# Kernel tuning notes

Hardware: AMD Instinct MI355X
Metric: run time of the kernel (lower is better)

## Reference

```python
import jax, jax.numpy as jnp
import numpy as np
import math

NB_STEPS = 50  # matches init kwarg nb_steps


def cc_quadrature(nb_steps):
    # Clenshaw-Curtis weights/nodes, identical to UMNN's compute_cc_weights.
    lam = np.arange(nb_steps + 1, dtype=np.float64).reshape(-1, 1)
    lam = np.cos((lam @ lam.T) * math.pi / nb_steps)
    lam[:, 0] = 0.5
    lam[:, -1] = 0.5 * lam[:, -1]
    lam = lam * 2.0 / nb_steps
    W = np.arange(nb_steps + 1, dtype=np.float64).reshape(-1, 1)
    W[np.arange(1, nb_steps + 1, 2)] = 0
    W = 2.0 / (1.0 - W ** 2)
    W[0] = 1
    W[np.arange(1, nb_steps + 1, 2)] = 0
    cc_weights = (lam.T @ W).astype(np.float32)                 # [K, 1]
    steps = np.cos(np.arange(nb_steps + 1, dtype=np.float64).reshape(-1, 1)
                   * math.pi / nb_steps).astype(np.float32)     # [K, 1]
    return jnp.asarray(cc_weights), jnp.asarray(steps)


def integrand_mlp(xh, W1, b1, W2, b2, W3, b3, W4, b4):
    y = jax.nn.relu(jnp.einsum('bkd,hd->bkh', xh, W1) + b1)
    y = jax.nn.relu(jnp.einsum('bkh,gh->bkg', y, W2) + b2)
    y = jax.nn.relu(jnp.einsum('bkg,fg->bkf', y, W3) + b3)
    y = jnp.einsum('bkf,of->bko', y, W4) + b4
    return jax.nn.elu(y) + 1.0


def setup_inputs() -> dict:
    key = jax.random.key(0)
    ks = jax.random.split(key, 10)
    B, HD, IN_D = 16384, 128, 64
    x = jax.random.normal(ks[0], (B, 1), dtype=jnp.float32)
    h = jax.random.normal(ks[1], (B, IN_D - 1), dtype=jnp.float32)
    def lin(k, fan_out, fan_in):
        return jax.random.normal(k, (fan_out, fan_in), dtype=jnp.float32) / np.sqrt(fan_in)
    return {
        'x': x, 'h': h,
        'W1': lin(ks[2], HD, IN_D), 'b1': jax.random.normal(ks[3], (HD,), dtype=jnp.float32) * 0.01,
        'W2': lin(ks[4], HD, HD),   'b2': jax.random.normal(ks[5], (HD,), dtype=jnp.float32) * 0.01,
        'W3': lin(ks[6], HD, HD),   'b3': jax.random.normal(ks[7], (HD,), dtype=jnp.float32) * 0.01,
        'W4': lin(ks[8], 1, HD),    'b4': jax.random.normal(ks[9], (1,), dtype=jnp.float32) * 0.01,
    }


def reference(x, h, W1, b1, W2, b2, W3, b3, W4, b4):
    cc_w, steps = cc_quadrature(NB_STEPS)          # [K,1], [K,1]
    xmax = jnp.max(x) + 10.0
    x0 = x                                          # [B,1]
    xT = jnp.zeros_like(x) + xmax                   # xfinal broadcast
    # quadrature points X_steps: [B, K, 1]
    X = x0[:, None, :] + (xT - x0)[:, None, :] * (steps[None, :, :] + 1.0) * 0.5
    B, K = X.shape[0], X.shape[1]
    hK = jnp.broadcast_to(h[:, None, :], (B, K, h.shape[1]))
    xh = jnp.concatenate([X, hK], axis=-1)          # [B, K, in_d]
    f = integrand_mlp(xh, W1, b1, W2, b2, W3, b3, W4, b4)  # [B, K, 1]
    z = jnp.sum(f * cc_w[None, :, :], axis=1)       # [B, 1]
    return z * (xT - x0) * 0.5
```

## Files before the change

### kernel.cpp

```cpp
#include <hip/hip_runtime.h>
#include <hip/hip_bf16.h>
#include <math.h>


#define B_N    16384
#define KQ     51
#define HD     128
#define IND    64
#define BLK    128
#define GRID   512
#define RPB    32
#define RPW    16
#define SPW    (RPW * KQ)
#define TPW    (SPW / 16)

typedef __attribute__((ext_vector_type(8))) short short8;
typedef __attribute__((ext_vector_type(4))) float f32x4;

union S8U { short8 s8; unsigned u[4]; };

__device__ __forceinline__ unsigned short f2bf(float f) {
    __hip_bfloat16 t = __float2bfloat16(f);
    return *reinterpret_cast<unsigned short*>(&t);
}

#if defined(__gfx950__) && defined(__has_builtin)
#if __has_builtin(__builtin_amdgcn_cvt_pk_bf16_f32)
#define HAVE_PK_BF16 1
#endif
#endif

__device__ __forceinline__ unsigned pk_bf16(float lo, float hi) {
#ifdef HAVE_PK_BF16
    typedef __attribute__((ext_vector_type(2))) __bf16 bfv2;
    bfv2 r = __builtin_amdgcn_cvt_pk_bf16_f32(lo, hi);
    return *reinterpret_cast<unsigned*>(&r);
#else
    return (unsigned)f2bf(lo) | ((unsigned)f2bf(hi) << 16);
#endif
}

__launch_bounds__(BLK, 1)
__global__ void umnn_fused(const float* __restrict__ x,  const float* __restrict__ h,
                           const float* __restrict__ W1, const float* __restrict__ b1,
                           const float* __restrict__ W2, const float* __restrict__ b2,
                           const float* __restrict__ W3, const float* __restrict__ b3,
                           const float* __restrict__ W4, const float* __restrict__ b4,
                           float* __restrict__ out)
{
    __shared__ __align__(16) float hpL[RPB * HD];
    __shared__ __align__(16) char  y2x[2][4096];
    __shared__ __align__(16) float hshT[63 * 36];
    __shared__ float vs[2][SPW + 16];
    __shared__ float xL[RPB];
    __shared__ float sSteps[KQ], sCcw[KQ];
    __shared__ float red2[2];

    const int tid  = threadIdx.x;
    const int w    = tid >> 6;
    const int lane = tid & 63;
    const int q    = lane >> 4;
    const int lm   = lane & 15;
    const int swz  = lm & 7;
    const int rowBase = blockIdx.x * RPB;

    if (tid < KQ) {
        const int j = tid;
        const float pi50 = 0.06283185307179586f;
        sSteps[j] = __cosf((float)j * pi50);
        float s = 0.0f;
        for (int i = 0; i <= 50; i += 2) {
            float Wi = (i == 0) ? 1.0f : 2.0f / (1.0f - (float)(i * i));
            float lam;
            if (j == 0) lam = 0.5f;
            else {
                int mp = (i * j) % 100;
                lam = __cosf((float)mp * pi50);
                if (j == 50) lam *= 0.5f;
            }
            s += (lam * 0.04f) * Wi;
        }
        sCcw[j] = s;
    }
    {
        const f32x4* x4 = (const f32x4*)x;
        float mx = -1e30f;
        for (int i = tid; i < B_N / 4; i += BLK) {
            f32x4 v = x4[i];
            mx = fmaxf(fmaxf(mx, fmaxf(v[0], v[1])), fmaxf(v[2], v[3]));
        }
        #pragma unroll
        for (int d = 32; d > 0; d >>= 1) mx = fmaxf(mx, __shfl_xor(mx, d));
        if (lane == 0) red2[w] = mx;
    }
    for (int i = tid; i < RPB * 63; i += BLK) {
        int r = i / 63, d = i - r * 63;
        hshT[d * 36 + r] = h[(rowBase) * 63 + i];
    }
    if (tid < RPB) xL[tid] = x[rowBase + tid];
    __syncthreads();

    const float xmax = fmaxf(red2[0], red2[1]) + 10.0f;

    {
        const int n = tid;
        float acc[RPB];
        const float b1v = b1[n];
        #pragma unroll
        for (int r = 0; r < RPB; ++r) acc[r] = b1v;
        const float* wr = W1 + n * IND + 1;
        #pragma unroll 1
        for (int d = 0; d < IND - 1; ++d) {
            float wv = wr[d];
            const float* ht = hshT + d * 36;
            #pragma unroll
            for (int rc = 0; rc < RPB / 4; ++rc) {
                f32x4 hv = *(const f32x4*)(ht + rc * 4);
                acc[rc * 4 + 0] = fmaf(wv, hv[0], acc[rc * 4 + 0]);
                acc[rc * 4 + 1] = fmaf(wv, hv[1], acc[rc * 4 + 1]);
                acc[rc * 4 + 2] = fmaf(wv, hv[2], acc[rc * 4 + 2]);
                acc[rc * 4 + 3] = fmaf(wv, hv[3], acc[rc * 4 + 3]);
            }
        }
        #pragma unroll
        for (int r = 0; r < RPB; ++r) hpL[r * HD + n] = acc[r];
    }

    float w1x[32];
    #pragma unroll
    for (int kk = 0; kk < 4; ++kk)
        #pragma unroll
        for (int j = 0; j < 8; ++j)
            w1x[kk * 8 + j] = W1[(kk * 32 + q * 8 + j) * IND];

    short8 W2A[8][4], W3A[8][4];
    f32x4  b2c[8], b3c[8], W4c[8];
    #pragma unroll
    for (int nt = 0; nt < 8; ++nt) {
        #pragma unroll
        for (int kk = 0; kk < 4; ++kk) {
            const float* p2 = W2 + (nt * 16 + lm) * HD + kk * 32 + q * 8;
            const float* p3 = W3 + (nt * 16 + lm) * HD + kk * 32 + q * 8;
            S8U a2, a3;
            #pragma unroll
            for (int j = 0; j < 4; ++j) {
                a2.u[j] = pk_bf16(p2[2 * j], p2[2 * j + 1]);
                a3.u[j] = pk_bf16(p3[2 * j], p3[2 * j + 1]);
            }
            W2A[nt][kk] = a2.s8; W3A[nt][kk] = a3.s8;
        }
        b2c[nt] = *(const f32x4*)(b2 + nt * 16 + q * 4);
        b3c[nt] = *(const f32x4*)(b3 + nt * 16 + q * 4);
        W4c[nt] = *(const f32x4*)(W4 + nt * 16 + q * 4);
    }
    const float b4v = b4[0];
    char*  myY2 = y2x[w];
    float* vsW  = vs[w];
    __syncthreads();

    const int S0 = blockIdx.x * (RPB * KQ) + w * SPW;

    auto computeY1 = [&](int tt, short8* Y) {
        const int s   = S0 + tt * 16 + lm;
        const unsigned row = (unsigned)s / KQ;
        const int k   = s - (int)row * KQ;
        const int rl  = min((int)row - rowBase, RPB - 1);
        const float x0 = xL[rl];
        const float X  = fmaf((xmax - x0) * 0.5f, sSteps[k] + 1.0f, x0);
        #pragma unroll
        for (int kk = 0; kk < 4; ++kk) {
            const float* hp = hpL + rl * HD + kk * 32 + q * 8;
            f32x4 ha = *(const f32x4*)hp;
            f32x4 hb = *(const f32x4*)(hp + 4);
            S8U u;
            u.u[0] = pk_bf16(fmaxf(fmaf(X, w1x[kk*8+0], ha[0]), 0.f),
                             fmaxf(fmaf(X, w1x[kk*8+1], ha[1]), 0.f));
            u.u[1] = pk_bf16(fmaxf(fmaf(X, w1x[kk*8+2], ha[2]), 0.f),
                             fmaxf(fmaf(X, w1x[kk*8+3], ha[3]), 0.f));
            u.u[2] = pk_bf16(fmaxf(fmaf(X, w1x[kk*8+4], hb[0]), 0.f),
                             fmaxf(fmaf(X, w1x[kk*8+5], hb[1]), 0.f));
            u.u[3] = pk_bf16(fmaxf(fmaf(X, w1x[kk*8+6], hb[2]), 0.f),
                             fmaxf(fmaf(X, w1x[kk*8+7], hb[3]), 0.f));
            Y[kk] = u.s8;
        }
    };

    short8 Y1c[4], Y1n[4];
    computeY1(0, Y1c);

    #pragma unroll 1
    for (int tt = 0; tt < TPW; ++tt) {
        f32x4 C[8];
        #pragma unroll
        for (int nt = 0; nt < 8; ++nt) C[nt] = b2c[nt];
        #pragma unroll
        for (int kk = 0; kk < 4; ++kk)
            #pragma unroll
            for (int nt = 0; nt < 8; ++nt)
                C[nt] = __builtin_amdgcn_mfma_f32_16x16x32_bf16(W2A[nt][kk], Y1c[kk], C[nt], 0, 0, 0);

        #pragma unroll
        for (int nt = 0; nt < 8; ++nt) {
            unsigned lo = pk_bf16(fmaxf(C[nt][0], 0.f), fmaxf(C[nt][1], 0.f));
            unsigned hi = pk_bf16(fmaxf(C[nt][2], 0.f), fmaxf(C[nt][3], 0.f));
            *(int2*)(myY2 + lm * 256 + (((2*nt + (q>>1)) ^ swz) << 4) + ((q & 1) << 3))
                = make_int2((int)lo, (int)hi);
        }

        computeY1(tt + 1, Y1n);

        short8 Y2[4];
        #pragma unroll
        for (int kk = 0; kk < 4; ++kk)
            Y2[kk] = *(const short8*)(myY2 + lm * 256 + (((kk*4 + q) ^ swz) << 4));

        #pragma unroll
        for (int nt = 0; nt < 8; ++nt) C[nt] = b3c[nt];
        #pragma unroll
        for (int kk = 0; kk < 4; ++kk)
            #pragma unroll
            for (int nt = 0; nt < 8; ++nt)
                C[nt] = __builtin_amdgcn_mfma_f32_16x16x32_bf16(W3A[nt][kk], Y2[kk], C[nt], 0, 0, 0);

        float p = 0.f;
        #pragma unroll
        for (int nt = 0; nt < 8; ++nt) {
            p = fmaf(fmaxf(C[nt][0], 0.f), W4c[nt][0], p);
            p = fmaf(fmaxf(C[nt][1], 0.f), W4c[nt][1], p);
            p = fmaf(fmaxf(C[nt][2], 0.f), W4c[nt][2], p);
            p = fmaf(fmaxf(C[nt][3], 0.f), W4c[nt][3], p);
        }
        p += __shfl_xor(p, 16);
        p += __shfl_xor(p, 32);
        if (lane < 16) vsW[tt * 16 + lm] = p;

        #pragma unroll
        for (int kk = 0; kk < 4; ++kk) Y1c[kk] = Y1n[kk];
    }

    {
        const int r   = lane >> 2;
        const int sub = lane & 3;
        float a = 0.f;
        #pragma unroll 1
        for (int j = 0; j < 13; ++j) {
            int k = sub + 4 * j;
            if (k < KQ) {
                float y4 = vsW[r * KQ + k] + b4v;
                float f  = (y4 > 0.f) ? (y4 + 1.f) : __expf(y4);
                a = fmaf(f, sCcw[k], a);
            }
        }
        a += __shfl_xor(a, 1);
        a += __shfl_xor(a, 2);
        if (sub == 0) {
            int rl = w * RPW + r;
            out[rowBase + rl] = a * (xmax - xL[rl]) * 0.5f;
        }
    }
}

extern "C" void kernel_launch(void* const* d_in, const int* in_sizes, int n_in,
                              void* d_out, int out_size, void* d_ws, size_t ws_size,
                              hipStream_t stream)
{
    const float* x  = (const float*)d_in[0];
    const float* h  = (const float*)d_in[1];
    const float* W1 = (const float*)d_in[2];
    const float* b1 = (const float*)d_in[3];
    const float* W2 = (const float*)d_in[4];
    const float* b2 = (const float*)d_in[5];
    const float* W3 = (const float*)d_in[6];
    const float* b3 = (const float*)d_in[7];
    const float* W4 = (const float*)d_in[8];
    const float* b4 = (const float*)d_in[9];
    float* out = (float*)d_out;

    umnn_fused<<<GRID, BLK, 0, stream>>>(x, h, W1, b1, W2, b2, W3, b3,
                                         W4, b4, out);
}
```

Measured before the change: 186.4 us.

## Split hidden dimension across waves, halve rows per block, double grid

Each block now handles 16 rows instead of 32, and the grid doubles to 1024 blocks. The two waves no longer each process their own rows. Instead they split the 128 output neurons of layers 2 and 3, each holding half of W2/W3 in registers. Y2 and the partial layer-4 sums are exchanged through shared memory with a __syncthreads per tile, and wave 0 does the final reduction. This halves register pressure so launch bounds allow 2 blocks per CU, but it adds a block-wide barrier per tile, drops the software-pipelined Y1 prefetch, and duplicates the Y1 computation across both waves.

```diff
diff --git a/kernel.cpp b/kernel.cpp
--- a/kernel.cpp
+++ b/kernel.cpp
@@ -8,11 +8,11 @@
 #define HD     128
 #define IND    64
 #define BLK    128
-#define GRID   512
-#define RPB    32
-#define RPW    16
-#define SPW    (RPW * KQ)
-#define TPW    (SPW / 16)
+#define GRID   1024
+#define RPB    16
+#define SPB    (RPB * KQ)
+#define TPB2   (SPB / 16)
+#define HPITCH 20
 
 typedef __attribute__((ext_vector_type(8))) short short8;
 typedef __attribute__((ext_vector_type(4))) float f32x4;
@@ -40,7 +40,7 @@
 #endif
 }
 
-__launch_bounds__(BLK, 1)
+__launch_bounds__(BLK, 2)
 __global__ void umnn_fused(const float* __restrict__ x,  const float* __restrict__ h,
                            const float* __restrict__ W1, const float* __restrict__ b1,
                            const float* __restrict__ W2, const float* __restrict__ b2,
@@ -49,9 +49,9 @@
                            float* __restrict__ out)
 {
     __shared__ __align__(16) float hpL[RPB * HD];
-    __shared__ __align__(16) char  y2x[2][4096];
-    __shared__ __align__(16) float hshT[63 * 36];
-    __shared__ float vs[2][SPW + 16];
+    __shared__ __align__(16) char  y2b[2][16 * 256];
+    __shared__ __align__(16) float hshT[63 * HPITCH];
+    __shared__ float vs[2][SPB];
     __shared__ float xL[RPB];
     __shared__ float sSteps[KQ], sCcw[KQ];
     __shared__ float red2[2];
@@ -95,7 +95,7 @@
     }
     for (int i = tid; i < RPB * 63; i += BLK) {
         int r = i / 63, d = i - r * 63;
-        hshT[d * 36 + r] = h[(rowBase) * 63 + i];
+        hshT[d * HPITCH + r] = h[rowBase * 63 + i];
     }
     if (tid < RPB) xL[tid] = x[rowBase + tid];
     __syncthreads();
@@ -112,7 +112,7 @@
         #pragma unroll 1
         for (int d = 0; d < IND - 1; ++d) {
             float wv = wr[d];
-            const float* ht = hshT + d * 36;
+            const float* ht = hshT + d * HPITCH;
             #pragma unroll
             for (int rc = 0; rc < RPB / 4; ++rc) {
                 f32x4 hv = *(const f32x4*)(ht + rc * 4);
@@ -133,14 +133,15 @@
         for (int j = 0; j < 8; ++j)
             w1x[kk * 8 + j] = W1[(kk * 32 + q * 8 + j) * IND];
 
-    short8 W2A[8][4], W3A[8][4];
-    f32x4  b2c[8], b3c[8], W4c[8];
+    short8 W2A[4][4], W3A[4][4];
+    f32x4  b2c[4], b3c[4], W4c[4];
     #pragma unroll
-    for (int nt = 0; nt < 8; ++nt) {
+    for (int nt = 0; nt < 4; ++nt) {
+        const int ntg = w * 4 + nt;
         #pragma unroll
         for (int kk = 0; kk < 4; ++kk) {
-            const float* p2 = W2 + (nt * 16 + lm) * HD + kk * 32 + q * 8;
-            const float* p3 = W3 + (nt * 16 + lm) * HD + kk * 32 + q * 8;
+            const float* p2 = W2 + (ntg * 16 + lm) * HD + kk * 32 + q * 8;
+            const float* p3 = W3 + (ntg * 16 + lm) * HD + kk * 32 + q * 8;
             S8U a2, a3;
             #pragma unroll
             for (int j = 0; j < 4; ++j) {
@@ -149,24 +150,27 @@
             }
             W2A[nt][kk] = a2.s8; W3A[nt][kk] = a3.s8;
         }
-        b2c[nt] = *(const f32x4*)(b2 + nt * 16 + q * 4);
-        b3c[nt] = *(const f32x4*)(b3 + nt * 16 + q * 4);
-        W4c[nt] = *(const f32x4*)(W4 + nt * 16 + q * 4);
+        b2c[nt] = *(const f32x4*)(b2 + ntg * 16 + q * 4);
+        b3c[nt] = *(const f32x4*)(b3 + ntg * 16 + q * 4);
+        W4c[nt] = *(const f32x4*)(W4 + ntg * 16 + q * 4);
     }
     const float b4v = b4[0];
-    char*  myY2 = y2x[w];
-    float* vsW  = vs[w];
+    float* vsW = vs[w];
     __syncthreads();
 
-    const int S0 = blockIdx.x * (RPB * KQ) + w * SPW;
-
-    auto computeY1 = [&](int tt, short8* Y) {
+    const int S0 = blockIdx.x * SPB;
+
+    #pragma unroll 1
+    for (int tt = 0; tt < TPB2; ++tt) {
+        char* buf = y2b[tt & 1];
+
         const int s   = S0 + tt * 16 + lm;
         const unsigned row = (unsigned)s / KQ;
         const int k   = s - (int)row * KQ;
-        const int rl  = min((int)row - rowBase, RPB - 1);
+        const int rl  = (int)row - rowBase;
         const float x0 = xL[rl];
         const float X  = fmaf((xmax - x0) * 0.5f, sSteps[k] + 1.0f, x0);
+        short8 Y1[4];
         #pragma unroll
         for (int kk = 0; kk < 4; ++kk) {
             const float* hp = hpL + rl * HD + kk * 32 + q * 8;
@@ -181,50 +185,43 @@
                              fmaxf(fmaf(X, w1x[kk*8+5], hb[1]), 0.f));
             u.u[3] = pk_bf16(fmaxf(fmaf(X, w1x[kk*8+6], hb[2]), 0.f),
                              fmaxf(fmaf(X, w1x[kk*8+7], hb[3]), 0.f));
-            Y[kk] = u.s8;
-        }
-    };
-
-    short8 Y1c[4], Y1n[4];
-    computeY1(0, Y1c);
-
-    #pragma unroll 1
-    for (int tt = 0; tt < TPW; ++tt) {
-        f32x4 C[8];
-        #pragma unroll
-        for (int nt = 0; nt < 8; ++nt) C[nt] = b2c[nt];
+            Y1[kk] = u.s8;
+        }
+
+        f32x4 C[4];
+        #pragma unroll
+        for (int nt = 0; nt < 4; ++nt) C[nt] = b2c[nt];
         #pragma unroll
         for (int kk = 0; kk < 4; ++kk)
             #pragma unroll
-            for (int nt = 0; nt < 8; ++nt)
-                C[nt] = __builtin_amdgcn_mfma_f32_16x16x32_bf16(W2A[nt][kk], Y1c[kk], C[nt], 0, 0, 0);
-
-        #pragma unroll
-        for (int nt = 0; nt < 8; ++nt) {
+            for (int nt = 0; nt < 4; ++nt)
+                C[nt] = __builtin_amdgcn_mfma_f32_16x16x32_bf16(W2A[nt][kk], Y1[kk], C[nt], 0, 0, 0);
+
+        #pragma unroll
+        for (int nt = 0; nt < 4; ++nt) {
+            const int cch = 2 * (w * 4 + nt) + (q >> 1);
             unsigned lo = pk_bf16(fmaxf(C[nt][0], 0.f), fmaxf(C[nt][1], 0.f));
             unsigned hi = pk_bf16(fmaxf(C[nt][2], 0.f), fmaxf(C[nt][3], 0.f));
-            *(int2*)(myY2 + lm * 256 + (((2*nt + (q>>1)) ^ swz) << 4) + ((q & 1) << 3))
+            *(int2*)(buf + lm * 256 + ((cch ^ swz) << 4) + ((q & 1) << 3))
                 = make_int2((int)lo, (int)hi);
         }
-
-        computeY1(tt + 1, Y1n);
+        __syncthreads();
 
         short8 Y2[4];
         #pragma unroll
         for (int kk = 0; kk < 4; ++kk)
-            Y2[kk] = *(const short8*)(myY2 + lm * 256 + (((kk*4 + q) ^ swz) << 4));
-
-        #pragma unroll
-        for (int nt = 0; nt < 8; ++nt) C[nt] = b3c[nt];
+            Y2[kk] = *(const short8*)(buf + lm * 256 + (((kk * 4 + q) ^ swz) << 4));
+        #pragma unroll
+        for (int nt = 0; nt < 4; ++nt) C[nt] = b3c[nt];
         #pragma unroll
         for (int kk = 0; kk < 4; ++kk)
             #pragma unroll
-            for (int nt = 0; nt < 8; ++nt)
+            for (int nt = 0; nt < 4; ++nt)
                 C[nt] = __builtin_amdgcn_mfma_f32_16x16x32_bf16(W3A[nt][kk], Y2[kk], C[nt], 0, 0, 0);
 
         float p = 0.f;
         #pragma unroll
-        for (int nt = 0; nt < 8; ++nt) {
+        for (int nt = 0; nt < 4; ++nt) {
             p = fmaf(fmaxf(C[nt][0], 0.f), W4c[nt][0], p);
             p = fmaf(fmaxf(C[nt][1], 0.f), W4c[nt][1], p);
             p = fmaf(fmaxf(C[nt][2], 0.f), W4c[nt][2], p);
@@ -233,12 +230,10 @@
         p += __shfl_xor(p, 16);
         p += __shfl_xor(p, 32);
         if (lane < 16) vsW[tt * 16 + lm] = p;
-
-        #pragma unroll
-        for (int kk = 0; kk < 4; ++kk) Y1c[kk] = Y1n[kk];
-    }
-
-    {
+    }
+    __syncthreads();
+
+    if (w == 0) {
         const int r   = lane >> 2;
         const int sub = lane & 3;
         float a = 0.f;
@@ -246,17 +241,16 @@
         for (int j = 0; j < 13; ++j) {
             int k = sub + 4 * j;
             if (k < KQ) {
-                float y4 = vsW[r * KQ + k] + b4v;
+                int sl = r * KQ + k;
+                float y4 = vs[0][sl] + vs[1][sl] + b4v;
                 float f  = (y4 > 0.f) ? (y4 + 1.f) : __expf(y4);
                 a = fmaf(f, sCcw[k], a);
             }
         }
         a += __shfl_xor(a, 1);
         a += __shfl_xor(a, 2);
-        if (sub == 0) {
-            int rl = w * RPW + r;
-            out[rowBase + rl] = a * (xmax - xL[rl]) * 0.5f;
-        }
+        if (sub == 0)
+            out[rowBase + r] = a * (xmax - xL[r]) * 0.5f;
     }
 }
 
```

After: 190.1 us. Within noise of the previous version (+2.0%).

## Use packed FMA for MLP math and defer cross-lane W4 reduction to epilogue

Applied to the files above, without the earlier changes.

Replaces scalar FMAs in the h·W1 precompute, the layer-1 X fan-in, and the final W4 dot product with v_pk_fma_f32 inline asm on float pairs. Removes the two per-tile shuffles by storing per-lane partial sums to shared memory, and sums the four quarter-wave partials in the final quadrature epilogue. The hshT buffer is aliased with the partial-sum buffer to save LDS, and swizzled Y2 addresses are precomputed once outside the loop. This costs extra LDS writes per tile and more registers for the packed values and offsets.

```diff
diff --git a/kernel.cpp b/kernel.cpp
--- a/kernel.cpp
+++ b/kernel.cpp
@@ -13,11 +13,19 @@
 #define RPW    16
 #define SPW    (RPW * KQ)
 #define TPW    (SPW / 16)
+#define HPITCH 36
 
 typedef __attribute__((ext_vector_type(8))) short short8;
 typedef __attribute__((ext_vector_type(4))) float f32x4;
+typedef __attribute__((ext_vector_type(2))) float f32x2;
 
 union S8U { short8 s8; unsigned u[4]; };
+
+__device__ __forceinline__ f32x2 pk_fma(f32x2 a, f32x2 b, f32x2 c) {
+    f32x2 d;
+    asm("v_pk_fma_f32 %0, %1, %2, %3" : "=v"(d) : "v"(a), "v"(b), "v"(c));
+    return d;
+}
 
 __device__ __forceinline__ unsigned short f2bf(float f) {
     __hip_bfloat16 t = __float2bfloat16(f);
@@ -50,11 +58,12 @@
 {
     __shared__ __align__(16) float hpL[RPB * HD];
     __shared__ __align__(16) char  y2x[2][4096];
-    __shared__ __align__(16) float hshT[63 * 36];
-    __shared__ float vs[2][SPW + 16];
+    __shared__ __align__(16) float uSh[2 * TPW * 64];
     __shared__ float xL[RPB];
     __shared__ float sSteps[KQ], sCcw[KQ];
     __shared__ float red2[2];
+
+    float* hshT = uSh;
 
     const int tid  = threadIdx.x;
     const int w    = tid >> 6;
@@ -95,7 +104,7 @@
     }
     for (int i = tid; i < RPB * 63; i += BLK) {
         int r = i / 63, d = i - r * 63;
-        hshT[d * 36 + r] = h[(rowBase) * 63 + i];
+        hshT[d * HPITCH + r] = h[rowBase * 63 + i];
     }
     if (tid < RPB) xL[tid] = x[rowBase + tid];
     __syncthreads();
@@ -104,37 +113,38 @@
 
     {
         const int n = tid;
-        float acc[RPB];
         const float b1v = b1[n];
-        #pragma unroll
-        for (int r = 0; r < RPB; ++r) acc[r] = b1v;
+        f32x2 acc2[RPB / 2];
+        #pragma unroll
+        for (int r = 0; r < RPB / 2; ++r) acc2[r] = (f32x2){b1v, b1v};
         const float* wr = W1 + n * IND + 1;
         #pragma unroll 1
         for (int d = 0; d < IND - 1; ++d) {
-            float wv = wr[d];
-            const float* ht = hshT + d * 36;
+            const float wv = wr[d];
+            const f32x2 wv2 = {wv, wv};
+            const float* ht = hshT + d * HPITCH;
             #pragma unroll
             for (int rc = 0; rc < RPB / 4; ++rc) {
                 f32x4 hv = *(const f32x4*)(ht + rc * 4);
-                acc[rc * 4 + 0] = fmaf(wv, hv[0], acc[rc * 4 + 0]);
-                acc[rc * 4 + 1] = fmaf(wv, hv[1], acc[rc * 4 + 1]);
-                acc[rc * 4 + 2] = fmaf(wv, hv[2], acc[rc * 4 + 2]);
-                acc[rc * 4 + 3] = fmaf(wv, hv[3], acc[rc * 4 + 3]);
+                acc2[rc * 2]     = pk_fma(wv2, (f32x2){hv[0], hv[1]}, acc2[rc * 2]);
+                acc2[rc * 2 + 1] = pk_fma(wv2, (f32x2){hv[2], hv[3]}, acc2[rc * 2 + 1]);
             }
         }
         #pragma unroll
-        for (int r = 0; r < RPB; ++r) hpL[r * HD + n] = acc[r];
-    }
-
-    float w1x[32];
+        for (int r = 0; r < RPB; ++r) hpL[r * HD + n] = acc2[r >> 1][r & 1];
+    }
+
+    f32x2 w1x2[16];
     #pragma unroll
     for (int kk = 0; kk < 4; ++kk)
         #pragma unroll
-        for (int j = 0; j < 8; ++j)
-            w1x[kk * 8 + j] = W1[(kk * 32 + q * 8 + j) * IND];
+        for (int jj = 0; jj < 4; ++jj)
+            w1x2[kk * 4 + jj] = (f32x2){W1[(kk * 32 + q * 8 + 2 * jj) * IND],
+                                        W1[(kk * 32 + q * 8 + 2 * jj + 1) * IND]};
 
     short8 W2A[8][4], W3A[8][4];
-    f32x4  b2c[8], b3c[8], W4c[8];
+    f32x4  b2c[8], b3c[8];
+    f32x2  W4c2[16];
     #pragma unroll
     for (int nt = 0; nt < 8; ++nt) {
         #pragma unroll
@@ -151,11 +161,20 @@
         }
         b2c[nt] = *(const f32x4*)(b2 + nt * 16 + q * 4);
         b3c[nt] = *(const f32x4*)(b3 + nt * 16 + q * 4);
-        W4c[nt] = *(const f32x4*)(W4 + nt * 16 + q * 4);
+        W4c2[nt * 2]     = *(const f32x2*)(W4 + nt * 16 + q * 4);
+        W4c2[nt * 2 + 1] = *(const f32x2*)(W4 + nt * 16 + q * 4 + 2);
     }
     const float b4v = b4[0];
     char*  myY2 = y2x[w];
-    float* vsW  = vs[w];
+    float* vsW  = uSh + w * (TPW * 64);
+
+    int wOff[8], rOff[4];
+    #pragma unroll
+    for (int nt = 0; nt < 8; ++nt)
+        wOff[nt] = lm * 256 + (((2 * nt + (q >> 1)) ^ swz) << 4) + ((q & 1) << 3);
+    #pragma unroll
+    for (int kk = 0; kk < 4; ++kk)
+        rOff[kk] = lm * 256 + (((kk * 4 + q) ^ swz) << 4);
     __syncthreads();
 
     const int S0 = blockIdx.x * (RPB * KQ) + w * SPW;
@@ -167,20 +186,21 @@
         const int rl  = min((int)row - rowBase, RPB - 1);
         const float x0 = xL[rl];
         const float X  = fmaf((xmax - x0) * 0.5f, sSteps[k] + 1.0f, x0);
+        const f32x2 X2 = {X, X};
         #pragma unroll
         for (int kk = 0; kk < 4; ++kk) {
             const float* hp = hpL + rl * HD + kk * 32 + q * 8;
             f32x4 ha = *(const f32x4*)hp;
             f32x4 hb = *(const f32x4*)(hp + 4);
+            f32x2 t0 = pk_fma(X2, w1x2[kk * 4 + 0], (f32x2){ha[0], ha[1]});
+            f32x2 t1 = pk_fma(X2, w1x2[kk * 4 + 1], (f32x2){ha[2], ha[3]});
+            f32x2 t2 = pk_fma(X2, w1x2[kk * 4 + 2], (f32x2){hb[0], hb[1]});
+            f32x2 t3 = pk_fma(X2, w1x2[kk * 4 + 3], (f32x2){hb[2], hb[3]});
             S8U u;
-            u.u[0] = pk_bf16(fmaxf(fmaf(X, w1x[kk*8+0], ha[0]), 0.f),
-                             fmaxf(fmaf(X, w1x[kk*8+1], ha[1]), 0.f));
-            u.u[1] = pk_bf16(fmaxf(fmaf(X, w1x[kk*8+2], ha[2]), 0.f),
-                             fmaxf(fmaf(X, w1x[kk*8+3], ha[3]), 0.f));
-            u.u[2] = pk_bf16(fmaxf(fmaf(X, w1x[kk*8+4], hb[0]), 0.f),
-                             fmaxf(fmaf(X, w1x[kk*8+5], hb[1]), 0.f));
-            u.u[3] = pk_bf16(fmaxf(fmaf(X, w1x[kk*8+6], hb[2]), 0.f),
-                             fmaxf(fmaf(X, w1x[kk*8+7], hb[3]), 0.f));
+            u.u[0] = pk_bf16(fmaxf(t0[0], 0.f), fmaxf(t0[1], 0.f));
+            u.u[1] = pk_bf16(fmaxf(t1[0], 0.f), fmaxf(t1[1], 0.f));
+            u.u[2] = pk_bf16(fmaxf(t2[0], 0.f), fmaxf(t2[1], 0.f));
+            u.u[3] = pk_bf16(fmaxf(t3[0], 0.f), fmaxf(t3[1], 0.f));
             Y[kk] = u.s8;
         }
     };
@@ -203,8 +223,7 @@
         for (int nt = 0; nt < 8; ++nt) {
             unsigned lo = pk_bf16(fmaxf(C[nt][0], 0.f), fmaxf(C[nt][1], 0.f));
             unsigned hi = pk_bf16(fmaxf(C[nt][2], 0.f), fmaxf(C[nt][3], 0.f));
-            *(int2*)(myY2 + lm * 256 + (((2*nt + (q>>1)) ^ swz) << 4) + ((q & 1) << 3))
-                = make_int2((int)lo, (int)hi);
+            *(int2*)(myY2 + wOff[nt]) = make_int2((int)lo, (int)hi);
         }
 
         computeY1(tt + 1, Y1n);
@@ -212,7 +231,7 @@
         short8 Y2[4];
         #pragma unroll
         for (int kk = 0; kk < 4; ++kk)
-            Y2[kk] = *(const short8*)(myY2 + lm * 256 + (((kk*4 + q) ^ swz) << 4));
+            Y2[kk] = *(const short8*)(myY2 + rOff[kk]);
 
         #pragma unroll
         for (int nt = 0; nt < 8; ++nt) C[nt] = b3c[nt];
@@ -222,17 +241,16 @@
             for (int nt = 0; nt < 8; ++nt)
                 C[nt] = __builtin_amdgcn_mfma_f32_16x16x32_bf16(W3A[nt][kk], Y2[kk], C[nt], 0, 0, 0);
 
-        float p = 0.f;
+        f32x2 acc = {0.f, 0.f};
         #pragma unroll
         for (int nt = 0; nt < 8; ++nt) {
-            p = fmaf(fmaxf(C[nt][0], 0.f), W4c[nt][0], p);
-            p = fmaf(fmaxf(C[nt][1], 0.f), W4c[nt][1], p);
-            p = fmaf(fmaxf(C[nt][2], 0.f), W4c[nt][2], p);
-            p = fmaf(fmaxf(C[nt][3], 0.f), W4c[nt][3], p);
-        }
-        p += __shfl_xor(p, 16);
-        p += __shfl_xor(p, 32);
-        if (lane < 16) vsW[tt * 16 + lm] = p;
+            f32x2 m0, m1;
+            m0[0] = fmaxf(C[nt][0], 0.f); m0[1] = fmaxf(C[nt][1], 0.f);
+            m1[0] = fmaxf(C[nt][2], 0.f); m1[1] = fmaxf(C[nt][3], 0.f);
+            acc = pk_fma(m0, W4c2[nt * 2],     acc);
+            acc = pk_fma(m1, W4c2[nt * 2 + 1], acc);
+        }
+        vsW[(tt << 6) + lane] = acc[0] + acc[1];
 
         #pragma unroll
         for (int kk = 0; kk < 4; ++kk) Y1c[kk] = Y1n[kk];
@@ -244,11 +262,14 @@
         float a = 0.f;
         #pragma unroll 1
         for (int j = 0; j < 13; ++j) {
-            int k = sub + 4 * j;
-            if (k < KQ) {
-                float y4 = vsW[r * KQ + k] + b4v;
+            int kq = sub + 4 * j;
+            if (kq < KQ) {
+                int sl   = r * KQ + kq;
+                int base = ((sl >> 4) << 6) + (sl & 15);
+                float y4 = vsW[base] + vsW[base + 16] + vsW[base + 32]
+                         + vsW[base + 48] + b4v;
                 float f  = (y4 > 0.f) ? (y4 + 1.f) : __expf(y4);
-                a = fmaf(f, sCcw[k], a);
+                a = fmaf(f, sCcw[kq], a);
             }
         }
         a += __shfl_xor(a, 1);
```

After: 193.1 us. 1.04x slower.
